# Optimization experiments

Measured on AMD Instinct MI355X. Metric: run time of the kernel, lower is better.

## Reference

```python
import jax, jax.numpy as jnp
import numpy as np

DIM, H, WH, WW = 192, 6, 8, 8
N = WH * WW
B = 4096
NW = 64
HALF = DIM // 2
HD = DIM // H


def _make_buffers():
    # continuous relative coords table (1, 2WH-1, 2WW-1, 2), Swin-V2 style
    rh = np.arange(-(WH - 1), WH, dtype=np.float32)
    rw = np.arange(-(WW - 1), WW, dtype=np.float32)
    gh, gw = np.meshgrid(rh, rw, indexing='ij')
    tab = np.stack([gh, gw], axis=-1)[None]  # (1, 2WH-1, 2WW-1, 2)
    tab[..., 0] /= WH - 1
    tab[..., 1] /= WW - 1
    tab *= 3.2
    tab = np.sign(tab) * (1.0 - np.exp(-np.abs(tab)))
    # relative position index (N, N) int
    ch, cw = np.meshgrid(np.arange(WH), np.arange(WW), indexing='ij')
    coords = np.stack([ch, cw]).reshape(2, -1)  # (2, N)
    rel = coords[:, :, None] - coords[:, None, :]  # (2, N, N)
    rel = rel.transpose(1, 2, 0).astype(np.int64)
    rel[:, :, 0] += WH - 1
    rel[:, :, 1] += WW - 1
    rel[:, :, 0] *= 2 * WW - 1
    idx = rel.sum(-1)  # (N, N)
    return jnp.asarray(tab, jnp.float32), jnp.asarray(idx, jnp.int32)


def setup_inputs() -> dict:
    key = jax.random.key(0)
    ks = jax.random.split(key, 24)
    w = lambda k, shape: jax.random.normal(k, shape, jnp.float32) * 0.02
    rpb_table, rp_index = _make_buffers()
    inp = {
        'x': jax.random.normal(ks[0], (B, N, DIM), jnp.float32),
        'mask': jnp.zeros((NW, N, N), jnp.float32),
        'logit_scale': jnp.log(10.0) * jnp.ones((H, 1, 1), jnp.float32),
        'mlp_w1': w(ks[1], (128, 2)), 'mlp_b1': jnp.zeros((128,), jnp.float32),
        'mlp_w2': w(ks[2], (H, 128)),
        'q1w': w(ks[3], (HALF, HALF)), 'q1b': jnp.zeros((HALF,), jnp.float32),
        'q2w': w(ks[4], (HALF, HALF)), 'q2b': jnp.zeros((HALF,), jnp.float32),
        'k1w': w(ks[5], (HALF, HALF)), 'k1b': jnp.zeros((HALF,), jnp.float32),
        'k2w': w(ks[6], (HALF, HALF)), 'k2b': jnp.zeros((HALF,), jnp.float32),
        'v1w': w(ks[7], (HALF, HALF)), 'v1b': jnp.zeros((HALF,), jnp.float32),
        'v2w': w(ks[8], (HALF, HALF)), 'v2b': jnp.zeros((HALF,), jnp.float32),
        'p1w': w(ks[9], (HALF, HALF)), 'p1b': jnp.zeros((HALF,), jnp.float32),
        'p2w': w(ks[10], (HALF, HALF)), 'p2b': jnp.zeros((HALF,), jnp.float32),
        'rpb_table': rpb_table,
        'rp_index': rp_index,
    }
    return inp


def _lin(x, w, b):
    return x @ w.T + b


def _l2n(x):
    return x / jnp.maximum(jnp.linalg.norm(x, axis=-1, keepdims=True), 1e-12)


def reference(x, mask, logit_scale, mlp_w1, mlp_b1, mlp_w2,
              q1w, q1b, q2w, q2b, k1w, k1b, k2w, k2b, v1w, v1b, v2w, v2b,
              p1w, p1b, p2w, p2b, rpb_table, rp_index):
    b, n, c = x.shape
    h, hd = H, c // H
    x0, x1 = x[..., :c // 2], x[..., c // 2:]
    # split-channel GRL residual projections, then concat halves -> heads
    def heads(y0w, y0b, y1w, y1b):
        y = jnp.concatenate([x0 + _lin(x0, y0w, y0b), x1 + _lin(x1, y1w, y1b)], -1)
        return y.reshape(b, n, h, hd).transpose(0, 2, 1, 3)  # (b, h, n, hd)
    q = heads(q1w, q1b, q2w, q2b)
    k = heads(k1w, k1b, k2w, k2b)
    v = heads(v1w, v1b, v2w, v2b)
    # cosine attention with learned per-head logit scale
    attn = jnp.einsum('bhnd,bhmd->bhnm', _l2n(q), _l2n(k))
    scale = jnp.exp(jnp.minimum(logit_scale, jnp.log(jnp.float32(100.0))))  # (h,1,1)
    attn = attn * scale
    # ESRPB: MLP over continuous relative coords -> per-head bias
    tab = jax.nn.relu(rpb_table @ mlp_w1.T + mlp_b1) @ mlp_w2.T  # (1, 2WH-1, 2WW-1, h)
    tab = tab.reshape(-1, h)
    rpb = tab[rp_index.reshape(-1)].reshape(n, n, h).transpose(2, 0, 1)  # (h, n, n)
    attn = attn + 16.0 * jax.nn.sigmoid(rpb)[None]
    nw = mask.shape[0]
    attn = (attn.reshape(b // nw, nw, h, n, n) + mask[None, :, None]).reshape(b, h, n, n)
    attn = jax.nn.softmax(attn, axis=-1)
    out = jnp.einsum('bhnm,bhmd->bhnd', attn, v).transpose(0, 2, 1, 3).reshape(b, n, c)
    o0, o1 = out[..., :c // 2], out[..., c // 2:]
    return jnp.concatenate([_lin(o0, p1w, p1b), _lin(o1, p2w, p2b)], -1)
```

## Files before the change

kernel.cpp:

```cpp
#include <hip/hip_runtime.h>
#include <hip/hip_bf16.h>

#define NT 64
#define DM 192

typedef __attribute__((ext_vector_type(4))) float f32x4;
typedef __attribute__((ext_vector_type(4))) float float4v;
using half2v = __attribute__((ext_vector_type(2))) _Float16;
using half4v = __attribute__((ext_vector_type(4))) _Float16;
using half8v = __attribute__((ext_vector_type(8))) _Float16;

#define BIAS_OFF  147456
#define TAB_OFF   6438912
#define SCALE_OFF 6444312

__device__ __forceinline__ half4v pk4(float a, float b, float c, float d){
  half2v lo = __builtin_bit_cast(half2v, __builtin_amdgcn_cvt_pkrtz(a, b));
  half2v hi = __builtin_bit_cast(half2v, __builtin_amdgcn_cvt_pkrtz(c, d));
  half4v r; r[0]=lo[0]; r[1]=lo[1]; r[2]=hi[0]; r[3]=hi[1];
  return r;
}

__global__ __launch_bounds__(384) void pre_a(
  const float* __restrict__ q1w, const float* __restrict__ q2w,
  const float* __restrict__ k1w, const float* __restrict__ k2w,
  const float* __restrict__ v1w, const float* __restrict__ v2w,
  const float* __restrict__ p1w, const float* __restrict__ p2w,
  const float* __restrict__ w1, const float* __restrict__ b1,
  const float* __restrict__ w2, const float* __restrict__ rpbt,
  const float* __restrict__ ls, char* __restrict__ ws)
{
  int blk = blockIdx.x, t = threadIdx.x;
  if (blk < 48) {
    const float* Ws[8] = {q1w,q2w,k1w,k2w,v1w,v2w,p1w,p2w};
    int mat = blk / 6, ct = blk % 6;
    int lane = t & 63, ks = t >> 6;
    if (ks < 3) {
      const float* W = Ws[mat];
      int c  = 16*ct + (lane & 15);
      int d0 = 32*ks + 8*(lane >> 4);
      half8v h;
      #pragma unroll
      for (int j = 0; j < 8; ++j) {
        float wel = W[c*96 + d0 + j];
        if (mat < 6 && c == d0 + j) wel += 1.0f;
        h[j] = (_Float16)wel;
      }
      *(half8v*)(ws + (size_t)((mat*6+ct)*3+ks)*1024 + lane*16) = h;
    }
  } else {
    float* tab = (float*)(ws + TAB_OFF);
    if (t < 225) {
      float t0 = rpbt[2*t], t1 = rpbt[2*t+1];
      float acc[6] = {0,0,0,0,0,0};
      for (int j = 0; j < 128; ++j) {
        float hv = fmaxf(t0*w1[2*j] + t1*w1[2*j+1] + b1[j], 0.f);
        #pragma unroll
        for (int hh = 0; hh < 6; ++hh) acc[hh] += hv * w2[hh*128 + j];
      }
      #pragma unroll
      for (int hh = 0; hh < 6; ++hh) tab[t*6 + hh] = acc[hh];
    }
    if (t >= 240 && t < 246) {
      float* sc = (float*)(ws + SCALE_OFF);
      int i = t - 240;
      sc[i] = expf(fminf(ls[i], 4.605170185988091f));
    }
  }
}

__global__ __launch_bounds__(256) void pre_b(
  const float* __restrict__ mask, const int* __restrict__ rpi,
  char* __restrict__ ws)
{
  int w = blockIdx.x / 6, h = blockIdx.x % 6;
  int lane = threadIdx.x & 63, nt = threadIdx.x >> 6;
  const float* tab = (const float*)(ws + TAB_OFF);
  float* bias = (float*)(ws + BIAS_OFF);
  #pragma unroll
  for (int mt = 0; mt < 4; ++mt)
    #pragma unroll
    for (int r = 0; r < 4; ++r) {
      int m = 16*mt + ((lane >> 4) << 2) + r;
      int n = 16*nt + (lane & 15);
      int idx = rpi[n*64 + m];
      float tv = tab[idx*6 + h];
      float sg = 16.f / (1.f + expf(-tv));
      float mv = mask[(w*64 + n)*64 + m];
      bias[(size_t)(((w*6+h)*4+mt)*4+nt)*256 + lane*4 + r] = sg + mv;
    }
}

__global__ __launch_bounds__(768, 2) void win_attn(
  const float* __restrict__ x, const char* __restrict__ ws,
  const float* __restrict__ q1b, const float* __restrict__ q2b,
  const float* __restrict__ k1b, const float* __restrict__ k2b,
  const float* __restrict__ v1b, const float* __restrict__ v2b,
  const float* __restrict__ p1b, const float* __restrict__ p2b,
  float* __restrict__ out)
{
  __shared__ __align__(16) _Float16 xo2[2][64*200];
  const int tid = threadIdx.x;
  const int wv = tid >> 6, lane = tid & 63;
  const int llo = lane & 15, lhi = lane >> 4;
  const int wgrp = (wv >= 6) ? 1 : 0;
  const int h = wv - 6*wgrp;
  const int b = blockIdx.x*2 + wgrp, w_in = b & 63;
  const int lt = tid - 384*wgrp;
  _Float16* xo = xo2[wgrp];
  const int half = (h < 3) ? 0 : 1;
  const int hd0 = 32 * (h % 3);
  const f32x4 zf = {0.f,0.f,0.f,0.f};
  const float* xg = x + (size_t)b * (NT*DM);

  float4v xv[8];
  #pragma unroll
  for (int it = 0; it < 8; ++it) xv[it] = *(const float4v*)(xg + 4*(lt + it*384));
  #pragma unroll
  for (int it = 0; it < 8; ++it) {
    int f4 = lt + it*384;
    int row = f4 / 48, c4 = f4 % 48;
    *(half4v*)(xo + row*200 + c4*4) = pk4(xv[it][0], xv[it][1], xv[it][2], xv[it][3]);
  }
  __syncthreads();

  const float scale_h = ((const float*)(ws + SCALE_OFF))[h];

  half4v qf[2][4], kf[2][4];
  {
    f32x4 qacc[2][4], kacc[2][4];
    #pragma unroll
    for (int dt = 0; dt < 2; ++dt)
      #pragma unroll
      for (int tt = 0; tt < 4; ++tt) { qacc[dt][tt] = zf; kacc[dt][tt] = zf; }
    __builtin_amdgcn_s_setprio(1);
    #pragma unroll
    for (int ks = 0; ks < 3; ++ks) {
      half8v xf[4];
      #pragma unroll
      for (int tt = 0; tt < 4; ++tt)
        xf[tt] = *(const half8v*)(xo + (16*tt+llo)*200 + half*96 + 32*ks + 8*lhi);
      #pragma unroll
      for (int dt = 0; dt < 2; ++dt) {
        half8v wq = *(const half8v*)(ws + (size_t)(((0+half)*6 + 2*(h%3)+dt)*3 + ks)*1024 + lane*16);
        half8v wk = *(const half8v*)(ws + (size_t)(((2+half)*6 + 2*(h%3)+dt)*3 + ks)*1024 + lane*16);
        #pragma unroll
        for (int tt = 0; tt < 4; ++tt) {
          qacc[dt][tt] = __builtin_amdgcn_mfma_f32_16x16x32_f16(wq, xf[tt], qacc[dt][tt], 0,0,0);
          kacc[dt][tt] = __builtin_amdgcn_mfma_f32_16x16x32_f16(wk, xf[tt], kacc[dt][tt], 0,0,0);
        }
      }
    }
    __builtin_amdgcn_s_setprio(0);
    const float* qbp = half ? q2b : q1b;
    const float* kbp = half ? k2b : k1b;
    float4v qb[2], kb[2];
    #pragma unroll
    for (int dt = 0; dt < 2; ++dt) {
      qb[dt] = *(const float4v*)(qbp + hd0 + 16*dt + 4*lhi);
      kb[dt] = *(const float4v*)(kbp + hd0 + 16*dt + 4*lhi);
    }
    #pragma unroll
    for (int tt = 0; tt < 4; ++tt) {
      float qv[2][4], kv[2][4];
      float sq = 0.f, sk = 0.f;
      #pragma unroll
      for (int dt = 0; dt < 2; ++dt)
        #pragma unroll
        for (int r = 0; r < 4; ++r) {
          qv[dt][r] = qacc[dt][tt][r] + qb[dt][r]; sq += qv[dt][r]*qv[dt][r];
          kv[dt][r] = kacc[dt][tt][r] + kb[dt][r]; sk += kv[dt][r]*kv[dt][r];
        }
      sq += __shfl_xor(sq, 16); sq += __shfl_xor(sq, 32);
      sk += __shfl_xor(sk, 16); sk += __shfl_xor(sk, 32);
      float invq = scale_h / fmaxf(sqrtf(sq), 1e-12f);
      float invk = 1.f / fmaxf(sqrtf(sk), 1e-12f);
      #pragma unroll
      for (int dt = 0; dt < 2; ++dt) {
        qf[dt][tt] = pk4(qv[dt][0]*invq, qv[dt][1]*invq, qv[dt][2]*invq, qv[dt][3]*invq);
        kf[dt][tt] = pk4(kv[dt][0]*invk, kv[dt][1]*invk, kv[dt][2]*invk, kv[dt][3]*invk);
      }
    }
  }

  const float4v* biasf = (const float4v*)(ws + BIAS_OFF);
  half4v pf[4][4];
  float inv_s[4];
  #pragma unroll
  for (int nt = 0; nt < 4; ++nt) {
    f32x4 s[4];
    #pragma unroll
    for (int mt = 0; mt < 4; ++mt) {
      f32x4 t0 = __builtin_amdgcn_mfma_f32_16x16x16f16(kf[0][mt], qf[0][nt], zf, 0,0,0);
      s[mt]    = __builtin_amdgcn_mfma_f32_16x16x16f16(kf[1][mt], qf[1][nt], t0, 0,0,0);
      float4v bb = biasf[(size_t)(((w_in*6 + h)*4 + mt)*4 + nt)*64 + lane];
      s[mt][0] += bb[0]; s[mt][1] += bb[1]; s[mt][2] += bb[2]; s[mt][3] += bb[3];
    }
    float mx = s[0][0];
    #pragma unroll
    for (int mt = 0; mt < 4; ++mt)
      #pragma unroll
      for (int r = 0; r < 4; ++r) mx = fmaxf(mx, s[mt][r]);
    mx = fmaxf(mx, __shfl_xor(mx, 16)); mx = fmaxf(mx, __shfl_xor(mx, 32));
    float e[4][4]; float sum = 0.f;
    #pragma unroll
    for (int mt = 0; mt < 4; ++mt)
      #pragma unroll
      for (int r = 0; r < 4; ++r) { e[mt][r] = __expf(s[mt][r] - mx); sum += e[mt][r]; }
    sum += __shfl_xor(sum, 16); sum += __shfl_xor(sum, 32);
    inv_s[nt] = 1.f / sum;
    #pragma unroll
    for (int mt = 0; mt < 4; ++mt)
      pf[mt][nt] = pk4(e[mt][0], e[mt][1], e[mt][2], e[mt][3]);
  }

  half4v vf[4][2];
  {
    f32x4 acc[4][2];
    #pragma unroll
    for (int tt = 0; tt < 4; ++tt) { acc[tt][0] = zf; acc[tt][1] = zf; }
    #pragma unroll
    for (int ks = 0; ks < 3; ++ks) {
      half8v xf[4];
      #pragma unroll
      for (int tt = 0; tt < 4; ++tt)
        xf[tt] = *(const half8v*)(xo + (16*tt+llo)*200 + half*96 + 32*ks + 8*lhi);
      #pragma unroll
      for (int ct = 0; ct < 2; ++ct) {
        half8v wvf = *(const half8v*)(ws + (size_t)(((4+half)*6 + 2*(h%3)+ct)*3 + ks)*1024 + lane*16);
        #pragma unroll
        for (int tt = 0; tt < 4; ++tt)
          acc[tt][ct] = __builtin_amdgcn_mfma_f32_16x16x32_f16(xf[tt], wvf, acc[tt][ct], 0,0,0);
      }
    }
    const float* vbp = half ? v2b : v1b;
    #pragma unroll
    for (int ct = 0; ct < 2; ++ct) {
      float vb = vbp[hd0 + 16*ct + llo];
      #pragma unroll
      for (int tt = 0; tt < 4; ++tt)
        vf[tt][ct] = pk4(acc[tt][ct][0] + vb, acc[tt][ct][1] + vb,
                         acc[tt][ct][2] + vb, acc[tt][ct][3] + vb);
    }
  }

  f32x4 oacc[2][4];
  #pragma unroll
  for (int dt = 0; dt < 2; ++dt)
    #pragma unroll
    for (int nt = 0; nt < 4; ++nt) oacc[dt][nt] = zf;
  __builtin_amdgcn_s_setprio(1);
  #pragma unroll
  for (int mt = 0; mt < 4; ++mt)
    #pragma unroll
    for (int dt = 0; dt < 2; ++dt)
      #pragma unroll
      for (int nt = 0; nt < 4; ++nt)
        oacc[dt][nt] = __builtin_amdgcn_mfma_f32_16x16x16f16(vf[mt][dt], pf[mt][nt], oacc[dt][nt], 0,0,0);
  __builtin_amdgcn_s_setprio(0);

  __syncthreads();
  #pragma unroll
  for (int dt = 0; dt < 2; ++dt)
    #pragma unroll
    for (int nt = 0; nt < 4; ++nt)
      *(half4v*)(xo + (16*nt+llo)*200 + 32*h + 16*dt + 4*lhi) =
        pk4(oacc[dt][nt][0]*inv_s[nt], oacc[dt][nt][1]*inv_s[nt],
            oacc[dt][nt][2]*inv_s[nt], oacc[dt][nt][3]*inv_s[nt]);
  __syncthreads();

  const int ph = h & 1;
  const int cp = h >> 1;
  f32x4 facc[2][4];
  #pragma unroll
  for (int cc = 0; cc < 2; ++cc)
    #pragma unroll
    for (int nt = 0; nt < 4; ++nt) facc[cc][nt] = zf;
  #pragma unroll
  for (int ks = 0; ks < 3; ++ks) {
    half8v of[4];
    #pragma unroll
    for (int nt = 0; nt < 4; ++nt)
      of[nt] = *(const half8v*)(xo + (16*nt+llo)*200 + 96*ph + 32*ks + 8*lhi);
    #pragma unroll
    for (int cc = 0; cc < 2; ++cc) {
      half8v wp = *(const half8v*)(ws + (size_t)(((6+ph)*6 + 2*cp+cc)*3 + ks)*1024 + lane*16);
      #pragma unroll
      for (int nt = 0; nt < 4; ++nt)
        facc[cc][nt] = __builtin_amdgcn_mfma_f32_16x16x32_f16(wp, of[nt], facc[cc][nt], 0,0,0);
    }
  }
  const float* pbp = ph ? p2b : p1b;
  float* og = out + (size_t)b * (NT*DM);
  #pragma unroll
  for (int cc = 0; cc < 2; ++cc) {
    float4v pb = *(const float4v*)(pbp + 16*(2*cp+cc) + 4*lhi);
    #pragma unroll
    for (int nt = 0; nt < 4; ++nt) {
      float4v res;
      #pragma unroll
      for (int r = 0; r < 4; ++r) res[r] = facc[cc][nt][r] + pb[r];
      *(float4v*)(og + (size_t)(16*nt+llo)*192 + 96*ph + 16*(2*cp+cc) + 4*lhi) = res;
    }
  }
}

extern "C" void kernel_launch(void* const* d_in, const int* in_sizes, int n_in,
                              void* d_out, int out_size, void* d_ws, size_t ws_size,
                              hipStream_t stream)
{
  const float* x    = (const float*)d_in[0];
  const float* mask = (const float*)d_in[1];
  const float* ls   = (const float*)d_in[2];
  const float* w1   = (const float*)d_in[3];
  const float* b1   = (const float*)d_in[4];
  const float* w2   = (const float*)d_in[5];
  const float* q1w  = (const float*)d_in[6];  const float* q1b = (const float*)d_in[7];
  const float* q2w  = (const float*)d_in[8];  const float* q2b = (const float*)d_in[9];
  const float* k1w  = (const float*)d_in[10]; const float* k1b = (const float*)d_in[11];
  const float* k2w  = (const float*)d_in[12]; const float* k2b = (const float*)d_in[13];
  const float* v1w  = (const float*)d_in[14]; const float* v1b = (const float*)d_in[15];
  const float* v2w  = (const float*)d_in[16]; const float* v2b = (const float*)d_in[17];
  const float* p1w  = (const float*)d_in[18]; const float* p1b = (const float*)d_in[19];
  const float* p2w  = (const float*)d_in[20]; const float* p2b = (const float*)d_in[21];
  const float* rpbt = (const float*)d_in[22];
  const int*   rpi  = (const int*)d_in[23];
  char* ws = (char*)d_ws;
  float* o = (float*)d_out;

  pre_a<<<49, 384, 0, stream>>>(q1w,q2w,k1w,k2w,v1w,v2w,p1w,p2w, w1,b1,w2, rpbt, ls, ws);
  pre_b<<<384, 256, 0, stream>>>(mask, rpi, ws);
  win_attn<<<2048, 768, 0, stream>>>(x, ws, q1b,q2b,k1b,k2b,v1b,v2b,p1b,p2b, o);
}
```

Measured before the change: 221.1 us.

## Make attention kernel persistent over 8 window pairs with double-buffered x prefetch

```diff
diff --git a/kernel.cpp b/kernel.cpp
--- a/kernel.cpp
+++ b/kernel.cpp
@@ -3,6 +3,7 @@
 
 #define NT 64
 #define DM 192
+#define NITER 8
 
 typedef __attribute__((ext_vector_type(4))) float f32x4;
 typedef __attribute__((ext_vector_type(4))) float float4v;
@@ -99,208 +100,233 @@
   const float* __restrict__ p1b, const float* __restrict__ p2b,
   float* __restrict__ out)
 {
-  __shared__ __align__(16) _Float16 xo2[2][64*200];
+  extern __shared__ char smem[];
+  _Float16* smh = (_Float16*)smem;
   const int tid = threadIdx.x;
   const int wv = tid >> 6, lane = tid & 63;
   const int llo = lane & 15, lhi = lane >> 4;
   const int wgrp = (wv >= 6) ? 1 : 0;
   const int h = wv - 6*wgrp;
-  const int b = blockIdx.x*2 + wgrp, w_in = b & 63;
   const int lt = tid - 384*wgrp;
-  _Float16* xo = xo2[wgrp];
+  const int bbase = blockIdx.x * (2*NITER);
   const int half = (h < 3) ? 0 : 1;
   const int hd0 = 32 * (h % 3);
   const f32x4 zf = {0.f,0.f,0.f,0.f};
-  const float* xg = x + (size_t)b * (NT*DM);
-
-  float4v xv[8];
-  #pragma unroll
-  for (int it = 0; it < 8; ++it) xv[it] = *(const float4v*)(xg + 4*(lt + it*384));
-  #pragma unroll
-  for (int it = 0; it < 8; ++it) {
-    int f4 = lt + it*384;
-    int row = f4 / 48, c4 = f4 % 48;
-    *(half4v*)(xo + row*200 + c4*4) = pk4(xv[it][0], xv[it][1], xv[it][2], xv[it][3]);
+  const float scale_h = ((const float*)(ws + SCALE_OFF))[h];
+  const float4v* biasf = (const float4v*)(ws + BIAS_OFF);
+
+
+  {
+    const float* xg = x + (size_t)(bbase + wgrp) * (NT*DM);
+    _Float16* xo = smh + (wgrp*2 + 0)*12800;
+    float4v xv[8];
+    #pragma unroll
+    for (int it = 0; it < 8; ++it) xv[it] = *(const float4v*)(xg + 4*(lt + it*384));
+    #pragma unroll
+    for (int it = 0; it < 8; ++it) {
+      int f4 = lt + it*384;
+      int row = f4 / 48, c4 = f4 % 48;
+      *(half4v*)(xo + row*200 + c4*4) = pk4(xv[it][0], xv[it][1], xv[it][2], xv[it][3]);
+    }
   }
   __syncthreads();
 
-  const float scale_h = ((const float*)(ws + SCALE_OFF))[h];
-
-  half4v qf[2][4], kf[2][4];
-  {
-    f32x4 qacc[2][4], kacc[2][4];
+  for (int i = 0; i < NITER; ++i) {
+    const int b = bbase + 2*i + wgrp;
+    const int w_in = b & 63;
+    _Float16* xo = smh + (wgrp*2 + (i&1))*12800;
+    _Float16* xn = smh + (wgrp*2 + ((i&1)^1))*12800;
+
+    half4v qf[2][4], kf[2][4];
+    {
+      f32x4 qacc[2][4], kacc[2][4];
+      #pragma unroll
+      for (int dt = 0; dt < 2; ++dt)
+        #pragma unroll
+        for (int tt = 0; tt < 4; ++tt) { qacc[dt][tt] = zf; kacc[dt][tt] = zf; }
+      __builtin_amdgcn_s_setprio(1);
+      #pragma unroll
+      for (int ks = 0; ks < 3; ++ks) {
+        half8v xf[4];
+        #pragma unroll
+        for (int tt = 0; tt < 4; ++tt)
+          xf[tt] = *(const half8v*)(xo + (16*tt+llo)*200 + half*96 + 32*ks + 8*lhi);
+        #pragma unroll
+        for (int dt = 0; dt < 2; ++dt) {
+          half8v wq = *(const half8v*)(ws + (size_t)(((0+half)*6 + 2*(h%3)+dt)*3 + ks)*1024 + lane*16);
+          half8v wk = *(const half8v*)(ws + (size_t)(((2+half)*6 + 2*(h%3)+dt)*3 + ks)*1024 + lane*16);
+          #pragma unroll
+          for (int tt = 0; tt < 4; ++tt) {
+            qacc[dt][tt] = __builtin_amdgcn_mfma_f32_16x16x32_f16(wq, xf[tt], qacc[dt][tt], 0,0,0);
+            kacc[dt][tt] = __builtin_amdgcn_mfma_f32_16x16x32_f16(wk, xf[tt], kacc[dt][tt], 0,0,0);
+          }
+        }
+      }
+      __builtin_amdgcn_s_setprio(0);
+      const float* qbp = half ? q2b : q1b;
+      const float* kbp = half ? k2b : k1b;
+      float4v qb[2], kb[2];
+      #pragma unroll
+      for (int dt = 0; dt < 2; ++dt) {
+        qb[dt] = *(const float4v*)(qbp + hd0 + 16*dt + 4*lhi);
+        kb[dt] = *(const float4v*)(kbp + hd0 + 16*dt + 4*lhi);
+      }
+      #pragma unroll
+      for (int tt = 0; tt < 4; ++tt) {
+        float qv[2][4], kv[2][4];
+        float sq = 0.f, sk = 0.f;
+        #pragma unroll
+        for (int dt = 0; dt < 2; ++dt)
+          #pragma unroll
+          for (int r = 0; r < 4; ++r) {
+            qv[dt][r] = qacc[dt][tt][r] + qb[dt][r]; sq += qv[dt][r]*qv[dt][r];
+            kv[dt][r] = kacc[dt][tt][r] + kb[dt][r]; sk += kv[dt][r]*kv[dt][r];
+          }
+        sq += __shfl_xor(sq, 16); sq += __shfl_xor(sq, 32);
+        sk += __shfl_xor(sk, 16); sk += __shfl_xor(sk, 32);
+        float invq = scale_h / fmaxf(sqrtf(sq), 1e-12f);
+        float invk = 1.f / fmaxf(sqrtf(sk), 1e-12f);
+        #pragma unroll
+        for (int dt = 0; dt < 2; ++dt) {
+          qf[dt][tt] = pk4(qv[dt][0]*invq, qv[dt][1]*invq, qv[dt][2]*invq, qv[dt][3]*invq);
+          kf[dt][tt] = pk4(kv[dt][0]*invk, kv[dt][1]*invk, kv[dt][2]*invk, kv[dt][3]*invk);
+        }
+      }
+    }
+
+    half4v pf[4][4];
+    float inv_s[4];
+    #pragma unroll
+    for (int nt = 0; nt < 4; ++nt) {
+      f32x4 s[4];
+      #pragma unroll
+      for (int mt = 0; mt < 4; ++mt) {
+        f32x4 t0 = __builtin_amdgcn_mfma_f32_16x16x16f16(kf[0][mt], qf[0][nt], zf, 0,0,0);
+        s[mt]    = __builtin_amdgcn_mfma_f32_16x16x16f16(kf[1][mt], qf[1][nt], t0, 0,0,0);
+        float4v bb = biasf[(size_t)(((w_in*6 + h)*4 + mt)*4 + nt)*64 + lane];
+        s[mt][0] += bb[0]; s[mt][1] += bb[1]; s[mt][2] += bb[2]; s[mt][3] += bb[3];
+      }
+      float mx = s[0][0];
+      #pragma unroll
+      for (int mt = 0; mt < 4; ++mt)
+        #pragma unroll
+        for (int r = 0; r < 4; ++r) mx = fmaxf(mx, s[mt][r]);
+      mx = fmaxf(mx, __shfl_xor(mx, 16)); mx = fmaxf(mx, __shfl_xor(mx, 32));
+      float e[4][4]; float sum = 0.f;
+      #pragma unroll
+      for (int mt = 0; mt < 4; ++mt)
+        #pragma unroll
+        for (int r = 0; r < 4; ++r) { e[mt][r] = __expf(s[mt][r] - mx); sum += e[mt][r]; }
+      sum += __shfl_xor(sum, 16); sum += __shfl_xor(sum, 32);
+      inv_s[nt] = 1.f / sum;
+      #pragma unroll
+      for (int mt = 0; mt < 4; ++mt)
+        pf[mt][nt] = pk4(e[mt][0], e[mt][1], e[mt][2], e[mt][3]);
+    }
+
+    float4v xvn[8];
+    if (i < NITER-1) {
+      const float* xgn = x + (size_t)(b + 2) * (NT*DM);
+      #pragma unroll
+      for (int it = 0; it < 8; ++it) xvn[it] = *(const float4v*)(xgn + 4*(lt + it*384));
+    }
+
+    half4v vf[4][2];
+    {
+      f32x4 acc[4][2];
+      #pragma unroll
+      for (int tt = 0; tt < 4; ++tt) { acc[tt][0] = zf; acc[tt][1] = zf; }
+      #pragma unroll
+      for (int ks = 0; ks < 3; ++ks) {
+        half8v xf[4];
+        #pragma unroll
+        for (int tt = 0; tt < 4; ++tt)
+          xf[tt] = *(const half8v*)(xo + (16*tt+llo)*200 + half*96 + 32*ks + 8*lhi);
+        #pragma unroll
+        for (int ct = 0; ct < 2; ++ct) {
+          half8v wvf = *(const half8v*)(ws + (size_t)(((4+half)*6 + 2*(h%3)+ct)*3 + ks)*1024 + lane*16);
+          #pragma unroll
+          for (int tt = 0; tt < 4; ++tt)
+            acc[tt][ct] = __builtin_amdgcn_mfma_f32_16x16x32_f16(xf[tt], wvf, acc[tt][ct], 0,0,0);
+        }
+      }
+      const float* vbp = half ? v2b : v1b;
+      #pragma unroll
+      for (int ct = 0; ct < 2; ++ct) {
+        float vb = vbp[hd0 + 16*ct + llo];
+        #pragma unroll
+        for (int tt = 0; tt < 4; ++tt)
+          vf[tt][ct] = pk4(acc[tt][ct][0] + vb, acc[tt][ct][1] + vb,
+                           acc[tt][ct][2] + vb, acc[tt][ct][3] + vb);
+      }
+    }
+
+    f32x4 oacc[2][4];
     #pragma unroll
     for (int dt = 0; dt < 2; ++dt)
       #pragma unroll
-      for (int tt = 0; tt < 4; ++tt) { qacc[dt][tt] = zf; kacc[dt][tt] = zf; }
+      for (int nt = 0; nt < 4; ++nt) oacc[dt][nt] = zf;
     __builtin_amdgcn_s_setprio(1);
     #pragma unroll
+    for (int mt = 0; mt < 4; ++mt)
+      #pragma unroll
+      for (int dt = 0; dt < 2; ++dt)
+        #pragma unroll
+        for (int nt = 0; nt < 4; ++nt)
+          oacc[dt][nt] = __builtin_amdgcn_mfma_f32_16x16x16f16(vf[mt][dt], pf[mt][nt], oacc[dt][nt], 0,0,0);
+    __builtin_amdgcn_s_setprio(0);
+
+    __syncthreads();
+    #pragma unroll
+    for (int dt = 0; dt < 2; ++dt)
+      #pragma unroll
+      for (int nt = 0; nt < 4; ++nt)
+        *(half4v*)(xo + (16*nt+llo)*200 + 32*h + 16*dt + 4*lhi) =
+          pk4(oacc[dt][nt][0]*inv_s[nt], oacc[dt][nt][1]*inv_s[nt],
+              oacc[dt][nt][2]*inv_s[nt], oacc[dt][nt][3]*inv_s[nt]);
+    if (i < NITER-1) {
+      #pragma unroll
+      for (int it = 0; it < 8; ++it) {
+        int f4 = lt + it*384;
+        int row = f4 / 48, c4 = f4 % 48;
+        *(half4v*)(xn + row*200 + c4*4) = pk4(xvn[it][0], xvn[it][1], xvn[it][2], xvn[it][3]);
+      }
+    }
+    __syncthreads();
+
+    const int ph = h & 1;
+    const int cp = h >> 1;
+    f32x4 facc[2][4];
+    #pragma unroll
+    for (int cc = 0; cc < 2; ++cc)
+      #pragma unroll
+      for (int nt = 0; nt < 4; ++nt) facc[cc][nt] = zf;
+    #pragma unroll
     for (int ks = 0; ks < 3; ++ks) {
-      half8v xf[4];
-      #pragma unroll
-      for (int tt = 0; tt < 4; ++tt)
-        xf[tt] = *(const half8v*)(xo + (16*tt+llo)*200 + half*96 + 32*ks + 8*lhi);
-      #pragma unroll
-      for (int dt = 0; dt < 2; ++dt) {
-        half8v wq = *(const half8v*)(ws + (size_t)(((0+half)*6 + 2*(h%3)+dt)*3 + ks)*1024 + lane*16);
-        half8v wk = *(const half8v*)(ws + (size_t)(((2+half)*6 + 2*(h%3)+dt)*3 + ks)*1024 + lane*16);
-        #pragma unroll
-        for (int tt = 0; tt < 4; ++tt) {
-          qacc[dt][tt] = __builtin_amdgcn_mfma_f32_16x16x32_f16(wq, xf[tt], qacc[dt][tt], 0,0,0);
-          kacc[dt][tt] = __builtin_amdgcn_mfma_f32_16x16x32_f16(wk, xf[tt], kacc[dt][tt], 0,0,0);
-        }
-      }
-    }
-    __builtin_amdgcn_s_setprio(0);
-    const float* qbp = half ? q2b : q1b;
-    const float* kbp = half ? k2b : k1b;
-    float4v qb[2], kb[2];
-    #pragma unroll
-    for (int dt = 0; dt < 2; ++dt) {
-      qb[dt] = *(const float4v*)(qbp + hd0 + 16*dt + 4*lhi);
-      kb[dt] = *(const float4v*)(kbp + hd0 + 16*dt + 4*lhi);
-    }
-    #pragma unroll
-    for (int tt = 0; tt < 4; ++tt) {
-      float qv[2][4], kv[2][4];
-      float sq = 0.f, sk = 0.f;
-      #pragma unroll
-      for (int dt = 0; dt < 2; ++dt)
-        #pragma unroll
-        for (int r = 0; r < 4; ++r) {
-          qv[dt][r] = qacc[dt][tt][r] + qb[dt][r]; sq += qv[dt][r]*qv[dt][r];
-          kv[dt][r] = kacc[dt][tt][r] + kb[dt][r]; sk += kv[dt][r]*kv[dt][r];
-        }
-      sq += __shfl_xor(sq, 16); sq += __shfl_xor(sq, 32);
-      sk += __shfl_xor(sk, 16); sk += __shfl_xor(sk, 32);
-      float invq = scale_h / fmaxf(sqrtf(sq), 1e-12f);
-      float invk = 1.f / fmaxf(sqrtf(sk), 1e-12f);
-      #pragma unroll
-      for (int dt = 0; dt < 2; ++dt) {
-        qf[dt][tt] = pk4(qv[dt][0]*invq, qv[dt][1]*invq, qv[dt][2]*invq, qv[dt][3]*invq);
-        kf[dt][tt] = pk4(kv[dt][0]*invk, kv[dt][1]*invk, kv[dt][2]*invk, kv[dt][3]*invk);
-      }
-    }
-  }
-
-  const float4v* biasf = (const float4v*)(ws + BIAS_OFF);
-  half4v pf[4][4];
-  float inv_s[4];
-  #pragma unroll
-  for (int nt = 0; nt < 4; ++nt) {
-    f32x4 s[4];
-    #pragma unroll
-    for (int mt = 0; mt < 4; ++mt) {
-      f32x4 t0 = __builtin_amdgcn_mfma_f32_16x16x16f16(kf[0][mt], qf[0][nt], zf, 0,0,0);
-      s[mt]    = __builtin_amdgcn_mfma_f32_16x16x16f16(kf[1][mt], qf[1][nt], t0, 0,0,0);
-      float4v bb = biasf[(size_t)(((w_in*6 + h)*4 + mt)*4 + nt)*64 + lane];
-      s[mt][0] += bb[0]; s[mt][1] += bb[1]; s[mt][2] += bb[2]; s[mt][3] += bb[3];
-    }
-    float mx = s[0][0];
-    #pragma unroll
-    for (int mt = 0; mt < 4; ++mt)
-      #pragma unroll
-      for (int r = 0; r < 4; ++r) mx = fmaxf(mx, s[mt][r]);
-    mx = fmaxf(mx, __shfl_xor(mx, 16)); mx = fmaxf(mx, __shfl_xor(mx, 32));
-    float e[4][4]; float sum = 0.f;
-    #pragma unroll
-    for (int mt = 0; mt < 4; ++mt)
-      #pragma unroll
-      for (int r = 0; r < 4; ++r) { e[mt][r] = __expf(s[mt][r] - mx); sum += e[mt][r]; }
-    sum += __shfl_xor(sum, 16); sum += __shfl_xor(sum, 32);
-    inv_s[nt] = 1.f / sum;
-    #pragma unroll
-    for (int mt = 0; mt < 4; ++mt)
-      pf[mt][nt] = pk4(e[mt][0], e[mt][1], e[mt][2], e[mt][3]);
-  }
-
-  half4v vf[4][2];
-  {
-    f32x4 acc[4][2];
-    #pragma unroll
-    for (int tt = 0; tt < 4; ++tt) { acc[tt][0] = zf; acc[tt][1] = zf; }
-    #pragma unroll
-    for (int ks = 0; ks < 3; ++ks) {
-      half8v xf[4];
-      #pragma unroll
-      for (int tt = 0; tt < 4; ++tt)
-        xf[tt] = *(const half8v*)(xo + (16*tt+llo)*200 + half*96 + 32*ks + 8*lhi);
-      #pragma unroll
-      for (int ct = 0; ct < 2; ++ct) {
-        half8v wvf = *(const half8v*)(ws + (size_t)(((4+half)*6 + 2*(h%3)+ct)*3 + ks)*1024 + lane*16);
-        #pragma unroll
-        for (int tt = 0; tt < 4; ++tt)
-          acc[tt][ct] = __builtin_amdgcn_mfma_f32_16x16x32_f16(xf[tt], wvf, acc[tt][ct], 0,0,0);
-      }
-    }
-    const float* vbp = half ? v2b : v1b;
-    #pragma unroll
-    for (int ct = 0; ct < 2; ++ct) {
-      float vb = vbp[hd0 + 16*ct + llo];
-      #pragma unroll
-      for (int tt = 0; tt < 4; ++tt)
-        vf[tt][ct] = pk4(acc[tt][ct][0] + vb, acc[tt][ct][1] + vb,
-                         acc[tt][ct][2] + vb, acc[tt][ct][3] + vb);
-    }
-  }
-
-  f32x4 oacc[2][4];
-  #pragma unroll
-  for (int dt = 0; dt < 2; ++dt)
-    #pragma unroll
-    for (int nt = 0; nt < 4; ++nt) oacc[dt][nt] = zf;
-  __builtin_amdgcn_s_setprio(1);
-  #pragma unroll
-  for (int mt = 0; mt < 4; ++mt)
-    #pragma unroll
-    for (int dt = 0; dt < 2; ++dt)
+      half8v of[4];
       #pragma unroll
       for (int nt = 0; nt < 4; ++nt)
-        oacc[dt][nt] = __builtin_amdgcn_mfma_f32_16x16x16f16(vf[mt][dt], pf[mt][nt], oacc[dt][nt], 0,0,0);
-  __builtin_amdgcn_s_setprio(0);
-
-  __syncthreads();
-  #pragma unroll
-  for (int dt = 0; dt < 2; ++dt)
-    #pragma unroll
-    for (int nt = 0; nt < 4; ++nt)
-      *(half4v*)(xo + (16*nt+llo)*200 + 32*h + 16*dt + 4*lhi) =
-        pk4(oacc[dt][nt][0]*inv_s[nt], oacc[dt][nt][1]*inv_s[nt],
-            oacc[dt][nt][2]*inv_s[nt], oacc[dt][nt][3]*inv_s[nt]);
-  __syncthreads();
-
-  const int ph = h & 1;
-  const int cp = h >> 1;
-  f32x4 facc[2][4];
-  #pragma unroll
-  for (int cc = 0; cc < 2; ++cc)
-    #pragma unroll
-    for (int nt = 0; nt < 4; ++nt) facc[cc][nt] = zf;
-  #pragma unroll
-  for (int ks = 0; ks < 3; ++ks) {
-    half8v of[4];
-    #pragma unroll
-    for (int nt = 0; nt < 4; ++nt)
-      of[nt] = *(const half8v*)(xo + (16*nt+llo)*200 + 96*ph + 32*ks + 8*lhi);
+        of[nt] = *(const half8v*)(xo + (16*nt+llo)*200 + 96*ph + 32*ks + 8*lhi);
+      #pragma unroll
+      for (int cc = 0; cc < 2; ++cc) {
+        half8v wp = *(const half8v*)(ws + (size_t)(((6+ph)*6 + 2*cp+cc)*3 + ks)*1024 + lane*16);
+        #pragma unroll
+        for (int nt = 0; nt < 4; ++nt)
+          facc[cc][nt] = __builtin_amdgcn_mfma_f32_16x16x32_f16(wp, of[nt], facc[cc][nt], 0,0,0);
+      }
+    }
+    const float* pbp = ph ? p2b : p1b;
+    float* og = out + (size_t)b * (NT*DM);
     #pragma unroll
     for (int cc = 0; cc < 2; ++cc) {
-      half8v wp = *(const half8v*)(ws + (size_t)(((6+ph)*6 + 2*cp+cc)*3 + ks)*1024 + lane*16);
-      #pragma unroll
-      for (int nt = 0; nt < 4; ++nt)
-        facc[cc][nt] = __builtin_amdgcn_mfma_f32_16x16x32_f16(wp, of[nt], facc[cc][nt], 0,0,0);
-    }
-  }
-  const float* pbp = ph ? p2b : p1b;
-  float* og = out + (size_t)b * (NT*DM);
-  #pragma unroll
-  for (int cc = 0; cc < 2; ++cc) {
-    float4v pb = *(const float4v*)(pbp + 16*(2*cp+cc) + 4*lhi);
-    #pragma unroll
-    for (int nt = 0; nt < 4; ++nt) {
-      float4v res;
-      #pragma unroll
-      for (int r = 0; r < 4; ++r) res[r] = facc[cc][nt][r] + pb[r];
-      *(float4v*)(og + (size_t)(16*nt+llo)*192 + 96*ph + 16*(2*cp+cc) + 4*lhi) = res;
+      float4v pb = *(const float4v*)(pbp + 16*(2*cp+cc) + 4*lhi);
+      #pragma unroll
+      for (int nt = 0; nt < 4; ++nt) {
+        float4v res;
+        #pragma unroll
+        for (int r = 0; r < 4; ++r) res[r] = facc[cc][nt][r] + pb[r];
+        *(float4v*)(og + (size_t)(16*nt+llo)*192 + 96*ph + 16*(2*cp+cc) + 4*lhi) = res;
+      }
     }
   }
 }
@@ -330,5 +356,8 @@
 
   pre_a<<<49, 384, 0, stream>>>(q1w,q2w,k1w,k2w,v1w,v2w,p1w,p2w, w1,b1,w2, rpbt, ls, ws);
   pre_b<<<384, 256, 0, stream>>>(mask, rpi, ws);
-  win_attn<<<2048, 768, 0, stream>>>(x, ws, q1b,q2b,k1b,k2b,v1b,v2b,p1b,p2b, o);
-}
+
+  hipFuncSetAttribute((const void*)win_attn,
+                      hipFuncAttributeMaxDynamicSharedMemorySize, 102400);
+  win_attn<<<256, 768, 102400, stream>>>(x, ws, q1b,q2b,k1b,k2b,v1b,v2b,p1b,p2b, o);
+}
```

Result: slower. 352.2 us (+59.3%).
